# Kernel tuning notes

Measured on AMD Instinct MI355X. Metric: run time of the kernel, lower is better.

Reference implementation:

```python
import jax, jax.numpy as jnp
import numpy as np
from jax import lax

# Dims from LSTMTagger class constants
B, S, LP = 1024, 128, 14       # sentences, words/sentence, padded chars/word
K, CE, WE, Lf = 3, 6, 10, 4    # char window, char emb, word emb, cnn filters
H, V, A, T = 6, 50000, 100, 135  # lstm hidden, vocab, alphabet, tagset
D = WE + Lf                     # lstm input dim = 14
LW = LP - K + 1                 # conv windows per word = 12


def setup_inputs() -> dict:
    key = jax.random.key(0)
    ks = jax.random.split(key, 14)
    n = lambda k, shp: jax.random.normal(k, shp, dtype=jnp.float32) * 0.1
    inp = {
        "word_idx": jax.random.randint(ks[0], (B, S), 0, V, dtype=jnp.int32),
        "char_idx": jax.random.randint(ks[1], (B, S, LP), 0, A, dtype=jnp.int32),
        "word_emb": n(ks[2], (V, WE)),
        "char_emb": n(ks[3], (A, CE)),
        "Wc": n(ks[4], (Lf, K * CE)),   # Conv1d(1, l, K*CE) weight, squeezed
        "bc": n(ks[5], (Lf,)),
        "Wih_f": n(ks[6], (4 * H, D)),
        "Whh_f": n(ks[7], (4 * H, H)),
        "b_f": n(ks[8], (4 * H,)),      # b_ih + b_hh fused (equivalent)
        "Wih_b": n(ks[9], (4 * H, D)),
        "Whh_b": n(ks[10], (4 * H, H)),
        "b_b": n(ks[11], (4 * H,)),
        "Wt": n(ks[12], (T, 2 * H)),
        "bt": n(ks[13], (T,)),
    }
    return inp


def _lstm_scan(xs, Wih, Whh, b):
    # xs: [S, B, D] -> hs: [S, B, H]; torch gate order i, f, g, o
    h0 = jnp.zeros((xs.shape[1], H), xs.dtype)

    def step(carry, xt):
        h, c = carry
        g = xt @ Wih.T + h @ Whh.T + b
        i, f, gg, o = jnp.split(g, 4, axis=-1)
        c = jax.nn.sigmoid(f) * c + jax.nn.sigmoid(i) * jnp.tanh(gg)
        h = jax.nn.sigmoid(o) * jnp.tanh(c)
        return (h, c), h

    _, hs = lax.scan(step, (h0, h0), xs)
    return hs


def reference(word_emb, char_emb, Wc, bc, Wih_f, Whh_f, b_f,
              Wih_b, Whh_b, b_b, Wt, bt, word_idx, char_idx):
    # per-word char CNN: sliding K-char windows, flatten, linear, max-pool
    ce = char_emb[char_idx]                              # [B,S,LP,CE]
    windows = jnp.concatenate([ce[:, :, i:i + LW] for i in range(K)], axis=-1)  # [B,S,LW,K*CE]
    phi = jnp.einsum('bswk,lk->bswl', windows, Wc) + bc  # [B,S,LW,Lf]
    char_repr = phi.max(axis=2)                          # [B,S,Lf]

    we = word_emb[word_idx]                              # [B,S,WE]
    x = jnp.concatenate([we, char_repr], axis=-1)        # [B,S,D]

    xs = x.transpose(1, 0, 2)                            # [S,B,D]
    hf = _lstm_scan(xs, Wih_f, Whh_f, b_f)               # forward direction
    hb = _lstm_scan(xs[::-1], Wih_b, Whh_b, b_b)[::-1]   # backward direction
    out = jnp.concatenate([hf, hb], axis=-1).transpose(1, 0, 2)  # [B,S,2H]

    tag_space = out @ Wt.T + bt                          # [B,S,T]
    return jax.nn.log_softmax(tag_space, axis=-1)
```

## Files before the change

### kernel.cpp

```cpp
#include <hip/hip_runtime.h>

#define B_   1024
#define S_   128
#define LP_  14
#define K_   3
#define CE_  6
#define WE_  10
#define LF_  4
#define H_   6
#define D_   14
#define T_   135
#define LW_  12
#define V_   50000
#define A_   100

static __device__ __forceinline__ float sigm(float x) {
    float e = __expf(-fabsf(x));
    float r = __frcp_rn(1.0f + e);
    return (x >= 0.f) ? r : e * r;
}
static __device__ __forceinline__ float tanh_(float x) {
    float e = __expf(-2.0f * fabsf(x));
    float r = (1.0f - e) * __frcp_rn(1.0f + e);
    return (x >= 0.f) ? r : -r;
}

__global__ __launch_bounds__(256) void k_el(
    const int* __restrict__ word_idx, const int* __restrict__ char_idx,
    const float* __restrict__ word_emb, const float* __restrict__ char_emb,
    const float* __restrict__ Wc, const float* __restrict__ bc,
    const float* __restrict__ Wih_f, const float* __restrict__ Whh_f, const float* __restrict__ b_f,
    const float* __restrict__ Wih_b, const float* __restrict__ Whh_b, const float* __restrict__ b_b,
    float* __restrict__ hbuf)
{
    __shared__ float s_x[512][16];
    __shared__ float s_h[4][S_][12];
    __shared__ float s_ce[A_ * CE_];
    __shared__ float s_wc[LF_ * K_ * CE_];
    __shared__ float s_bc[LF_];

    int t = threadIdx.x;
    for (int e = t; e < A_ * CE_; e += 256) s_ce[e] = char_emb[e];
    if (t < LF_ * K_ * CE_) s_wc[t] = Wc[t];
    if (t < LF_) s_bc[t] = bc[t];
    __syncthreads();

    int Wbase = blockIdx.x * 512;
    #pragma unroll
    for (int rep = 0; rep < 2; ++rep) {
        int wl = t + rep * 256;
        int w  = Wbase + wl;
        const int2* ci2 = (const int2*)(char_idx + (size_t)w * LP_);
        int idxs[LP_];
        #pragma unroll
        for (int p = 0; p < 7; ++p) {
            int2 v = ci2[p];
            idxs[2 * p] = v.x; idxs[2 * p + 1] = v.y;
        }
        float ce[LP_][CE_];
        #pragma unroll
        for (int p = 0; p < LP_; ++p) {
            int idx = idxs[p];
            idx = idx < 0 ? 0 : (idx >= A_ ? A_ - 1 : idx);
            #pragma unroll
            for (int c = 0; c < CE_; ++c) ce[p][c] = s_ce[idx * CE_ + c];
        }
        float xr[16];
        #pragma unroll
        for (int l = 0; l < LF_; ++l) {
            float acc[LW_];
            float bl = s_bc[l];
            #pragma unroll
            for (int q = 0; q < LW_; ++q) acc[q] = bl;
            #pragma unroll
            for (int kk = 0; kk < K_; ++kk) {
                #pragma unroll
                for (int c = 0; c < CE_; ++c) {
                    float wv_ = s_wc[l * (K_ * CE_) + kk * CE_ + c];
                    #pragma unroll
                    for (int q = 0; q < LW_; ++q) acc[q] = fmaf(ce[q + kk][c], wv_, acc[q]);
                }
            }
            float m = acc[0];
            #pragma unroll
            for (int q = 1; q < LW_; ++q) m = fmaxf(m, acc[q]);
            xr[WE_ + l] = m;
        }
        int wi = word_idx[w];
        wi = wi < 0 ? 0 : (wi >= V_ ? V_ - 1 : wi);
        const float2* wep = (const float2*)(word_emb + (size_t)wi * WE_);
        #pragma unroll
        for (int c = 0; c < WE_ / 2; ++c) {
            float2 v = wep[c];
            xr[2 * c] = v.x; xr[2 * c + 1] = v.y;
        }
        xr[14] = 0.f; xr[15] = 0.f;
        float4* xp = (float4*)&s_x[wl][0];
        xp[0] = make_float4(xr[0], xr[1], xr[2], xr[3]);
        xp[1] = make_float4(xr[4], xr[5], xr[6], xr[7]);
        xp[2] = make_float4(xr[8], xr[9], xr[10], xr[11]);
        xp[3] = make_float4(xr[12], xr[13], xr[14], xr[15]);
    }
    __syncthreads();

    int wv   = t >> 6;
    int lane = t & 63;
    int dir  = lane >> 5;
    int l    = lane & 31;
    bool act = (l < 24);
    int u = act ? (l % 6) : 0;
    int j = act ? (l / 6) : 0;
    int base = dir << 5;
    bool isg = (j == 2);

    {
        const float* Wih = dir ? Wih_b : Wih_f;
        const float* Whh = dir ? Whh_b : Whh_f;
        const float* bi  = dir ? b_b  : b_f;
        int r = j * H_ + u;
        float wih[D_], whh[H_], bias;
        #pragma unroll
        for (int k = 0; k < D_; ++k) wih[k] = Wih[r * D_ + k];
        #pragma unroll
        for (int k = 0; k < H_; ++k) whh[k] = Whh[r * H_ + k];
        bias = bi[r];

        float h[H_];
        #pragma unroll
        for (int k = 0; k < H_; ++k) h[k] = 0.f;
        float c = 0.f;

        float ax = bias;
        {
            const float* xp = &s_x[wv * S_ + (dir ? S_ - 1 : 0)][0];
            #pragma unroll
            for (int k = 0; k < D_; ++k) ax = fmaf(wih[k], xp[k], ax);
        }
        for (int s = 0; s < S_; ++s) {
            int se = dir ? (S_ - 1 - s) : s;
            float a = ax;
            #pragma unroll
            for (int k = 0; k < H_; ++k) a = fmaf(whh[k], h[k], a);
            float xx = isg ? (a + a) : a;
            float sg = sigm(xx);
            float ac = isg ? fmaf(2.f, sg, -1.f) : sg;
            float vi = __shfl(ac, base + u,      64);
            float vf = __shfl(ac, base + u + 6,  64);
            float vg = __shfl(ac, base + u + 12, 64);
            float vo = __shfl(ac, base + u + 18, 64);
            c = fmaf(vf, c, vi * vg);
            float hu = vo * tanh_(c);
            if (act && j == 0) s_h[wv][se][dir * H_ + u] = hu;
            #pragma unroll
            for (int k = 0; k < H_; ++k) h[k] = __shfl(hu, base + k, 64);
            if (s + 1 < S_) {
                const float* xp = &s_x[wv * S_ + (dir ? S_ - 2 - s : s + 1)][0];
                float t2 = bias;
                #pragma unroll
                for (int k = 0; k < D_; ++k) t2 = fmaf(wih[k], xp[k], t2);
                ax = t2;
            }
        }
    }
    __syncthreads();

    {
        float4* dst = (float4*)(hbuf + (size_t)blockIdx.x * 4 * S_ * 12);
        const float4* src = (const float4*)&s_h[0][0][0];
        #pragma unroll
        for (int i = 0; i < 6; ++i) dst[t + 256 * i] = src[t + 256 * i];
    }
}

__global__ __launch_bounds__(256) void k_p(
    const float* __restrict__ hbuf,
    const float* __restrict__ Wt, const float* __restrict__ bt,
    float* __restrict__ out)
{
    __shared__ float s_hb[64 * 12];
    int t = threadIdx.x;
    int ib = blockIdx.x * 64;
    {
        const float4* src = (const float4*)(hbuf + (size_t)ib * 12);
        float4* dst = (float4*)s_hb;
        if (t < 192) dst[t] = src[t];
    }
    __syncthreads();

    int lane = t & 63, wv = t >> 6;
    bool has2 = (lane < T_ - 128);
    int t2c = has2 ? (lane + 128) : (T_ - 1);

    float wA[12], wB[12], wC[12];
    #pragma unroll
    for (int jj = 0; jj < 12; ++jj) {
        wA[jj] = Wt[lane * 12 + jj];
        wB[jj] = Wt[(lane + 64) * 12 + jj];
        wC[jj] = Wt[t2c * 12 + jj];
    }
    float bA = bt[lane], bB = bt[lane + 64], bC = bt[t2c];

    int it0 = wv * 16;
    #pragma unroll 4
    for (int k = 0; k < 16; ++k) {
        int it = it0 + k;
        const float4* h4 = (const float4*)(s_hb + it * 12);
        float4 a0 = h4[0], a1 = h4[1], a2 = h4[2];
        float hv[12] = {a0.x, a0.y, a0.z, a0.w, a1.x, a1.y, a1.z, a1.w, a2.x, a2.y, a2.z, a2.w};
        float y0 = bA, y1 = bB, y2 = bC;
        #pragma unroll
        for (int jj = 0; jj < 12; ++jj) {
            y0 = fmaf(hv[jj], wA[jj], y0);
            y1 = fmaf(hv[jj], wB[jj], y1);
            y2 = fmaf(hv[jj], wC[jj], y2);
        }
        float ss = __expf(y0) + __expf(y1) + (has2 ? __expf(y2) : 0.0f);
        #pragma unroll
        for (int mk = 1; mk < 64; mk <<= 1) ss += __shfl_xor(ss, mk, 64);
        float ls = __logf(ss);
        float* op = out + (size_t)(ib + it) * T_;
        op[lane]      = y0 - ls;
        op[lane + 64] = y1 - ls;
        if (has2) op[lane + 128] = y2 - ls;
    }
}

extern "C" void kernel_launch(void* const* d_in, const int* in_sizes, int n_in,
                              void* d_out, int out_size, void* d_ws, size_t ws_size,
                              hipStream_t stream)
{
    const int* word_idx = (const int*)d_in[0];
    const int* char_idx = (const int*)d_in[1];
    const float* word_emb = (const float*)d_in[2];
    const float* char_emb = (const float*)d_in[3];
    const float* Wc    = (const float*)d_in[4];
    const float* bc    = (const float*)d_in[5];
    const float* Wih_f = (const float*)d_in[6];
    const float* Whh_f = (const float*)d_in[7];
    const float* b_f   = (const float*)d_in[8];
    const float* Wih_b = (const float*)d_in[9];
    const float* Whh_b = (const float*)d_in[10];
    const float* b_b   = (const float*)d_in[11];
    const float* Wt    = (const float*)d_in[12];
    const float* bt    = (const float*)d_in[13];

    float* hbuf = (float*)d_ws;

    k_el<<<B_ / 4, 256, 0, stream>>>(word_idx, char_idx, word_emb, char_emb, Wc, bc,
                                     Wih_f, Whh_f, b_f, Wih_b, Whh_b, b_b, hbuf);
    k_p<<<(B_ * S_) / 64, 256, 0, stream>>>(hbuf, Wt, bt, (float*)d_out);
}
```

Baseline: 163.0 us.

## Precompute LSTM input gates in parallel and compute all four gates per lane

```diff
diff --git a/kernel.cpp b/kernel.cpp
--- a/kernel.cpp
+++ b/kernel.cpp
@@ -14,15 +14,11 @@
 #define V_   50000
 #define A_   100
 
-static __device__ __forceinline__ float sigm(float x) {
-    float e = __expf(-fabsf(x));
-    float r = __frcp_rn(1.0f + e);
-    return (x >= 0.f) ? r : e * r;
-}
-static __device__ __forceinline__ float tanh_(float x) {
-    float e = __expf(-2.0f * fabsf(x));
-    float r = (1.0f - e) * __frcp_rn(1.0f + e);
-    return (x >= 0.f) ? r : -r;
+static __device__ __forceinline__ float fsigm(float x) {
+    return __frcp_rn(1.0f + __expf(-x));
+}
+static __device__ __forceinline__ float ftanh(float x) {
+    return fmaf(2.0f, __frcp_rn(1.0f + __expf(-2.0f * x)), -1.0f);
 }
 
 __global__ __launch_bounds__(256) void k_el(
@@ -33,7 +29,7 @@
     const float* __restrict__ Wih_b, const float* __restrict__ Whh_b, const float* __restrict__ b_b,
     float* __restrict__ hbuf)
 {
-    __shared__ float s_x[512][16];
+    __shared__ float s_g[4][S_][49];
     __shared__ float s_h[4][S_][12];
     __shared__ float s_ce[A_ * CE_];
     __shared__ float s_wc[LF_ * K_ * CE_];
@@ -49,7 +45,10 @@
     #pragma unroll
     for (int rep = 0; rep < 2; ++rep) {
         int wl = t + rep * 256;
+        int sent = wl >> 7;
+        int step = wl & (S_ - 1);
         int w  = Wbase + wl;
+
         const int2* ci2 = (const int2*)(char_idx + (size_t)w * LP_);
         int idxs[LP_];
         #pragma unroll
@@ -65,7 +64,7 @@
             #pragma unroll
             for (int c = 0; c < CE_; ++c) ce[p][c] = s_ce[idx * CE_ + c];
         }
-        float xr[16];
+        float x[D_];
         #pragma unroll
         for (int l = 0; l < LF_; ++l) {
             float acc[LW_];
@@ -84,7 +83,7 @@
             float m = acc[0];
             #pragma unroll
             for (int q = 1; q < LW_; ++q) m = fmaxf(m, acc[q]);
-            xr[WE_ + l] = m;
+            x[WE_ + l] = m;
         }
         int wi = word_idx[w];
         wi = wi < 0 ? 0 : (wi >= V_ ? V_ - 1 : wi);
@@ -92,73 +91,79 @@
         #pragma unroll
         for (int c = 0; c < WE_ / 2; ++c) {
             float2 v = wep[c];
-            xr[2 * c] = v.x; xr[2 * c + 1] = v.y;
-        }
-        xr[14] = 0.f; xr[15] = 0.f;
-        float4* xp = (float4*)&s_x[wl][0];
-        xp[0] = make_float4(xr[0], xr[1], xr[2], xr[3]);
-        xp[1] = make_float4(xr[4], xr[5], xr[6], xr[7]);
-        xp[2] = make_float4(xr[8], xr[9], xr[10], xr[11]);
-        xp[3] = make_float4(xr[12], xr[13], xr[14], xr[15]);
-    }
-    __syncthreads();
-
-    int wv   = t >> 6;
-    int lane = t & 63;
-    int dir  = lane >> 5;
-    int l    = lane & 31;
-    bool act = (l < 24);
-    int u = act ? (l % 6) : 0;
-    int j = act ? (l / 6) : 0;
-    int base = dir << 5;
-    bool isg = (j == 2);
+            x[2 * c] = v.x; x[2 * c + 1] = v.y;
+        }
+
+        #pragma unroll
+        for (int r = 0; r < 4 * H_; ++r) {
+            float a = b_f[r];
+            #pragma unroll
+            for (int k = 0; k < D_; ++k) a = fmaf(Wih_f[r * D_ + k], x[k], a);
+            s_g[sent][step][r] = a;
+        }
+        #pragma unroll
+        for (int r = 0; r < 4 * H_; ++r) {
+            float a = b_b[r];
+            #pragma unroll
+            for (int k = 0; k < D_; ++k) a = fmaf(Wih_b[r * D_ + k], x[k], a);
+            s_g[sent][step][24 + r] = a;
+        }
+    }
+    __syncthreads();
 
     {
-        const float* Wih = dir ? Wih_b : Wih_f;
+        int wv2  = t >> 6;
+        int lane = t & 63;
+        int dir  = lane >> 5;
+        int l    = lane & 31;
+        bool act = (l < H_);
+        int u    = act ? l : (H_ - 1);
+
         const float* Whh = dir ? Whh_b : Whh_f;
-        const float* bi  = dir ? b_b  : b_f;
-        int r = j * H_ + u;
-        float wih[D_], whh[H_], bias;
-        #pragma unroll
-        for (int k = 0; k < D_; ++k) wih[k] = Wih[r * D_ + k];
-        #pragma unroll
-        for (int k = 0; k < H_; ++k) whh[k] = Whh[r * H_ + k];
-        bias = bi[r];
-
-        float h[H_];
-        #pragma unroll
-        for (int k = 0; k < H_; ++k) h[k] = 0.f;
+        float whh[4][H_];
+        #pragma unroll
+        for (int j = 0; j < 4; ++j)
+            #pragma unroll
+            for (int k = 0; k < H_; ++k)
+                whh[j][k] = Whh[(j * H_ + u) * H_ + k];
+
+        const float* gp = &s_g[wv2][dir ? (S_ - 1) : 0][dir * 24 + u];
+        int gstride = dir ? -49 : 49;
+
+        float hv[H_];
+        #pragma unroll
+        for (int k = 0; k < H_; ++k) hv[k] = 0.f;
         float c = 0.f;
 
-        float ax = bias;
-        {
-            const float* xp = &s_x[wv * S_ + (dir ? S_ - 1 : 0)][0];
-            #pragma unroll
-            for (int k = 0; k < D_; ++k) ax = fmaf(wih[k], xp[k], ax);
-        }
+        float g0 = gp[0], g1 = gp[6], g2 = gp[12], g3 = gp[18];
         for (int s = 0; s < S_; ++s) {
+            float ai = g0, af = g1, ag = g2, ao = g3;
+            if (s + 1 < S_) {
+                gp += gstride;
+                g0 = gp[0]; g1 = gp[6]; g2 = gp[12]; g3 = gp[18];
+            }
+            #pragma unroll
+            for (int k = 0; k < H_; ++k) {
+                ai = fmaf(whh[0][k], hv[k], ai);
+                af = fmaf(whh[1][k], hv[k], af);
+                ag = fmaf(whh[2][k], hv[k], ag);
+                ao = fmaf(whh[3][k], hv[k], ao);
+            }
+            float si = fsigm(ai);
+            float sf = fsigm(af);
+            float so = fsigm(ao);
+            float tg = ftanh(ag);
+            c = fmaf(sf, c, si * tg);
+            float hu = so * ftanh(c);
+
             int se = dir ? (S_ - 1 - s) : s;
-            float a = ax;
-            #pragma unroll
-            for (int k = 0; k < H_; ++k) a = fmaf(whh[k], h[k], a);
-            float xx = isg ? (a + a) : a;
-            float sg = sigm(xx);
-            float ac = isg ? fmaf(2.f, sg, -1.f) : sg;
-            float vi = __shfl(ac, base + u,      64);
-            float vf = __shfl(ac, base + u + 6,  64);
-            float vg = __shfl(ac, base + u + 12, 64);
-            float vo = __shfl(ac, base + u + 18, 64);
-            c = fmaf(vf, c, vi * vg);
-            float hu = vo * tanh_(c);
-            if (act && j == 0) s_h[wv][se][dir * H_ + u] = hu;
-            #pragma unroll
-            for (int k = 0; k < H_; ++k) h[k] = __shfl(hu, base + k, 64);
-            if (s + 1 < S_) {
-                const float* xp = &s_x[wv * S_ + (dir ? S_ - 2 - s : s + 1)][0];
-                float t2 = bias;
-                #pragma unroll
-                for (int k = 0; k < D_; ++k) t2 = fmaf(wih[k], xp[k], t2);
-                ax = t2;
+            if (act) s_h[wv2][se][dir * H_ + u] = hu;
+
+            #pragma unroll
+            for (int k = 0; k < H_; ++k) {
+                int vf = __builtin_amdgcn_readlane(__float_as_int(hu), k);
+                int vb = __builtin_amdgcn_readlane(__float_as_int(hu), 32 + k);
+                hv[k] = __int_as_float(dir ? vb : vf);
             }
         }
     }
```

After: 186.9 us. 1.15x slower.
